# Kernel optimization log

Hardware: AMD Instinct MI355X
Metric: run time of the kernel (lower is better)

The kernel has to match this reference:

```python
import jax, jax.numpy as jnp
import numpy as np

N_NODES = 200000
E = 100000
H = 128            # hidden_dim = memory_dim = time_dim
EF = 64            # edge_feat_dim (raw_msg_dim)
L = 50             # price_seq_dim
LH = 32            # LSTM hidden size
MSG_DIM = EF + 2 * H + H  # IdentityMessage output = 448
N_PARTIES, N_STATES = 8, 56


def setup_inputs() -> dict:
    key = jax.random.key(0)
    ks = jax.random.split(key, 32)
    f = lambda k, shp, s=0.05: jax.random.normal(k, shp, dtype=jnp.float32) * s
    return {
        "src": jax.random.randint(ks[0], (E,), 0, N_NODES),
        "dst": jax.random.randint(ks[1], (E,), 0, N_NODES),
        "t": jnp.sort(jax.random.randint(ks[2], (E,), 0, 1000000)),
        "msg": jax.random.normal(ks[3], (E, EF), dtype=jnp.float32),
        "price_seq": jax.random.normal(ks[4], (E, L), dtype=jnp.float32),
        "trade_t": jax.random.randint(ks[5], (E,), 0, 1000000),
        "x_static": jax.random.randint(ks[6], (N_NODES, 2), 0, N_PARTIES),
        # TGN memory state
        "memory": f(ks[7], (N_NODES, H), 0.1),
        "last_update": jax.random.uniform(ks[8], (N_NODES,), dtype=jnp.float32) * 1000.0,
        # time encoder: cos(Linear(dt))
        "w_t": f(ks[9], (H,), 0.01),
        "b_t": f(ks[10], (H,)),
        # GRUCell memory updater
        "W_ih": f(ks[11], (3 * H, MSG_DIM)),
        "b_ih": f(ks[12], (3 * H,)),
        "W_hh": f(ks[13], (3 * H, H)),
        "b_hh": f(ks[14], (3 * H,)),
        # static embeddings + projection
        "party_emb": f(ks[15], (N_PARTIES, 16), 1.0),
        "state_emb": f(ks[16], (N_STATES, 16), 1.0),
        "W_sp": f(ks[17], (H, 32)),
        "b_sp": f(ks[18], (H,)),
        # price LSTM (input_size=1, hidden=32)
        "W_ih_l": f(ks[19], (4 * LH, 1)),
        "W_hh_l": f(ks[20], (4 * LH, LH)),
        "b_ih_l": f(ks[21], (4 * LH,)),
        "b_hh_l": f(ks[22], (4 * LH,)),
        "W_pp": f(ks[23], (H, LH)),
        "b_pp": f(ks[24], (H,)),
        # predictor MLP (dropout inactive at inference)
        "W1": f(ks[25], (64, 3 * H)),
        "b1": f(ks[26], (64,)),
        "W2": f(ks[27], (1, 64)),
        "b2": f(ks[28], (1,)),
    }


def reference(src, dst, t, msg, price_seq, trade_t, x_static, memory, last_update,
              w_t, b_t, W_ih, b_ih, W_hh, b_hh, party_emb, state_emb, W_sp, b_sp,
              W_ih_l, W_hh_l, b_ih_l, b_hh_l, W_pp, b_pp, W1, b1, W2, b2):
    N, Hd = memory.shape
    tf = t.astype(jnp.float32)
    t_enc = lambda dt: jnp.cos(dt[:, None] * w_t[None, :] + b_t[None, :])

    # ---- TGNMemory.update_state: gather -> message -> last-aggregate -> GRU scatter ----
    mem_s, mem_d = memory[src], memory[dst]
    msg_s = jnp.concatenate([mem_s, mem_d, msg, t_enc(tf - last_update[src])], axis=-1)
    msg_d = jnp.concatenate([mem_d, mem_s, msg, t_enc(tf - last_update[dst])], axis=-1)
    msgs = jnp.concatenate([msg_s, msg_d], axis=0)        # [2E, MSG_DIM]
    idx = jnp.concatenate([src, dst])                     # [2E]
    te = jnp.concatenate([tf, tf])
    M = idx.shape[0]
    # LastAggregator: per node, keep the message with the largest t (ties -> later event)
    perm = jnp.argsort(te)                                # stable ascending
    ranks = jnp.zeros((M,), jnp.int32).at[perm].set(jnp.arange(M, dtype=jnp.int32))
    win_rank = jax.ops.segment_max(ranks, idx, num_segments=N)  # int32 min for empty segs
    has_msg = win_rank >= 0
    win = perm[jnp.clip(win_rank, 0, M - 1)]
    agg = jnp.where(has_msg[:, None], msgs[win], 0.0)     # [N, MSG_DIM]
    # GRUCell update (applied only to nodes with messages)
    gi = agg @ W_ih.T + b_ih
    gh = memory @ W_hh.T + b_hh
    ir, iz, inn = jnp.split(gi, 3, axis=-1)
    hr, hz, hn = jnp.split(gh, 3, axis=-1)
    r = jax.nn.sigmoid(ir + hr)
    z = jax.nn.sigmoid(iz + hz)
    n = jnp.tanh(inn + r * hn)
    mem_new = jnp.where(has_msg[:, None], (1.0 - z) * n + z * memory, memory)

    # ---- static embeddings ----
    sf = jnp.concatenate([party_emb[x_static[src, 0]], state_emb[x_static[src, 1]]], axis=1)
    src_static = sf @ W_sp.T + b_sp

    # ---- price LSTM (input_size=1) ----
    B = price_seq.shape[0]
    nLH = W_hh_l.shape[1]
    bias = b_ih_l + b_hh_l

    def step(carry, x_t):
        h, c = carry
        g = x_t[:, None] * W_ih_l[:, 0][None, :] + h @ W_hh_l.T + bias
        i, fg, gg, o = jnp.split(g, 4, axis=-1)
        c = jax.nn.sigmoid(fg) * c + jax.nn.sigmoid(i) * jnp.tanh(gg)
        h = jax.nn.sigmoid(o) * jnp.tanh(c)
        return (h, c), None

    h0 = jnp.zeros((B, nLH), price_seq.dtype)
    (h_n, _), _ = jax.lax.scan(step, (h0, h0), price_seq.T)
    price_emb = h_n @ W_pp.T + b_pp

    # ---- fuse contexts + predictor MLP (dropout = identity at eval) ----
    combined = jnp.concatenate([mem_new[src] + src_static,
                                mem_new[dst] + price_emb,
                                price_emb], axis=1)
    h1 = jax.nn.relu(combined @ W1.T + b1)
    return (h1 @ W2.T + b2)[:, 0]
```

## Files before the change

### kernel.cpp

```cpp
#include <hip/hip_runtime.h>
#include <stdint.h>

#define NN    200000
#define NE    100000
#define HD    128
#define EFD   64
#define NG    384

typedef unsigned long long u64;
typedef short bf16x8 __attribute__((ext_vector_type(8)));
typedef float f32x4  __attribute__((ext_vector_type(4)));

#define OFF_KEY   ((size_t)0)
#define OFF_CNT   ((size_t)1600000)
#define OFF_LIST  ((size_t)1600256)
#define OFF_UV    ((size_t)2400256)
#define OFF_HN    ((size_t)104800256)
#define OFF_A     ((size_t)117600256)
#define OFF_B     ((size_t)117608448)
#define OFF_C0    ((size_t)117616640)
#define OFF_WBF   ((size_t)117616896)
#define WS_NEED   ((size_t)118092032)

#define W1OFF 221184

__device__ __forceinline__ float frcp(float x){ return __builtin_amdgcn_rcpf(x); }
__device__ __forceinline__ float sigf(float x){ return frcp(1.f + __expf(-x)); }
__device__ __forceinline__ float tanhf_(float x){ return 1.f - 2.f*frcp(__expf(2.f*x) + 1.f); }
__device__ __forceinline__ float4 ld4(const float* p){ return *reinterpret_cast<const float4*>(p); }

__device__ __forceinline__ short f2bf(float f){
  unsigned u = __float_as_uint(f);
  u += 0x7fffu + ((u>>16)&1u);
  return (short)(u>>16);
}

__device__ __forceinline__ unsigned cvtpk(float lo, float hi){
  unsigned r;
  asm("v_cvt_pk_bf16_f32 %0, %1, %2" : "=v"(r) : "v"(lo), "v"(hi));
  return r;
}

__device__ __forceinline__ void gl16(const void* g, void* l) {
  __builtin_amdgcn_global_load_lds(
      (const __attribute__((address_space(1))) void*)g,
      (__attribute__((address_space(3))) void*)l, 16, 0, 0);
}

__global__ void k_scatter(const int* __restrict__ src, const int* __restrict__ dst,
                          const int* __restrict__ t, u64* __restrict__ key) {
  int e = blockIdx.x*256 + threadIdx.x;
  if (e >= NE) return;
  u64 tt = (u64)(unsigned)(t[e] + 1);
  atomicMax(&key[src[e]], (tt<<18) | (u64)(unsigned)e);
  atomicMax(&key[dst[e]], (tt<<18) | (1ULL<<17) | (u64)(unsigned)e);
}

__global__ void k_compact(const u64* __restrict__ key, int* __restrict__ list,
                          int* __restrict__ count) {
  int n = blockIdx.x*256 + threadIdx.x;
  if (n >= NN) return;
  if (key[n] != 0ULL) { int p = atomicAdd(count, 1); list[p] = n; }
}

__global__ void k_pre(const float* __restrict__ W1, const float* __restrict__ W_sp,
                      const float* __restrict__ W_pp, const float* __restrict__ b_sp,
                      const float* __restrict__ b_pp, const float* __restrict__ b1,
                      float* __restrict__ A, float* __restrict__ B, float* __restrict__ c0)
{
  int tid = blockIdx.x*256 + threadIdx.x;
  if (tid < 2048) {
    int o = tid >> 5, j = tid & 31;
    float s = 0.f;
    for (int k = 0; k < 128; ++k) s = fmaf(W1[o*NG + k], W_sp[k*32 + j], s);
    A[tid] = s;
  } else if (tid < 4096) {
    int q = tid - 2048;
    int o = q >> 5, j = q & 31;
    float s = 0.f;
    for (int k = 0; k < 128; ++k)
      s = fmaf(W1[o*NG + 128 + k] + W1[o*NG + 256 + k], W_pp[k*32 + j], s);
    B[q] = s;
  } else if (tid < 4160) {
    int o = tid - 4096;
    float s = b1[o];
    for (int k = 0; k < 128; ++k) {
      s = fmaf(W1[o*NG + k], b_sp[k], s);
      s = fmaf(W1[o*NG + 128 + k] + W1[o*NG + 256 + k], b_pp[k], s);
    }
    c0[o] = s;
  }
}

__global__ void k_prew(const float* __restrict__ W_ih, const float* __restrict__ W_hh,
                       const float* __restrict__ W1, short* __restrict__ Wbf)
{
  int idx = blockIdx.x*256 + threadIdx.x;
  if (idx < 9*384*8) {
    int s   = idx & 7;
    int n   = (idx >> 3) % 384;
    int ch9 = idx / (384*8);
    int k8  = s ^ (n & 7);
    int k   = ch9*64 + k8*8;
    short v[8];
    #pragma unroll
    for (int e = 0; e < 8; ++e) {
      int kk = k + e;
      float f = (kk < 448) ? W_ih[(size_t)n*448 + kk] : W_hh[(size_t)n*HD + (kk-448)];
      v[e] = f2bf(f);
    }
    *reinterpret_cast<bf16x8*>(Wbf + (size_t)ch9*24576 + n*64 + s*8) =
        *reinterpret_cast<bf16x8*>(v);
  } else if (idx < 9*384*8 + 128*16) {
    int idx2 = idx - 9*384*8;
    int s = idx2 & 15, r = idx2 >> 4;
    int k8 = s ^ (r & 15);
    int k = k8*8;
    short v[8];
    #pragma unroll
    for (int e = 0; e < 8; ++e) {
      int kk = k + e;
      float f = (r < 64) ? W1[(size_t)r*NG + kk] : W1[(size_t)(r-64)*NG + 128 + kk];
      v[e] = f2bf(f);
    }
    *reinterpret_cast<bf16x8*>(Wbf + W1OFF + r*128 + s*8) =
        *reinterpret_cast<bf16x8*>(v);
  }
}

__global__ __launch_bounds__(512, 2) void k_gru(
    const u64* __restrict__ key, const int* __restrict__ list, const int* __restrict__ count,
    const int* __restrict__ src, const int* __restrict__ dst, const int* __restrict__ t,
    const float* __restrict__ msg, const float* __restrict__ memory,
    const float* __restrict__ last_update,
    const float* __restrict__ w_t, const float* __restrict__ b_t,
    const short* __restrict__ Wbf, const float* __restrict__ b_ih,
    const float* __restrict__ b_hh, float* __restrict__ uv)
{
  __shared__ short Wsb[24576];
  __shared__ short Xsb[4096];
  __shared__ float bias4[512];
  __shared__ int   sn_self[64];
  __shared__ int   sn_other[64];
  __shared__ int   sn_e[64];
  __shared__ float sn_dt[64];

  short* Mn2 = &Wsb[16384];

  int cnt = count[0];
  int base = blockIdx.x * 64;
  if (base >= cnt) return;
  int tid = threadIdx.x;
  int wid = tid >> 6, lane = tid & 63;
  int lr = lane & 15, lk = lane >> 4;

  if (tid < 64) {
    int idx = base + tid;
    int cl = idx < cnt ? idx : (cnt - 1);
    int n = list[cl];
    u64 k = key[n];
    int e   = (int)(k & 0x1FFFFULL);
    int isd = (int)((k >> 17) & 1ULL);
    sn_self[tid]  = n;
    sn_other[tid] = isd ? src[e] : dst[e];
    sn_e[tid]     = e;
    sn_dt[tid]    = (float)t[e] - last_update[n];
  }
  if (tid < 128) {
    int h = tid;
    bias4[h]       = b_ih[h]       + b_hh[h];
    bias4[128 + h] = b_ih[128 + h] + b_hh[128 + h];
    bias4[256 + h] = b_ih[256 + h];
    bias4[384 + h] = b_hh[256 + h];
  }
  __syncthreads();

  f32x4 aR[4], aZ[4], aNX[4], aNM[4];
  #pragma unroll
  for (int mt = 0; mt < 4; ++mt) { aR[mt] = (f32x4)0.f; aZ[mt] = (f32x4)0.f;
                                   aNX[mt] = (f32x4)0.f; aNM[mt] = (f32x4)0.f; }

  int node8 = tid >> 3, k8s = tid & 7;

  float4 xA0, xB0, xA1, xB1, xA2, xB2, xA3, xB3, xA4, xB4;
  {
    const float* pSelf  = memory + (size_t)sn_self[node8]*HD  + k8s*8;
    const float* pOther = memory + (size_t)sn_other[node8]*HD + k8s*8;
    const float* pMsg   = msg + (size_t)sn_e[node8]*EFD + k8s*8;
    xA0 = ld4(pSelf);       xB0 = ld4(pSelf+4);
    xA1 = ld4(pSelf+64);    xB1 = ld4(pSelf+68);
    xA2 = ld4(pOther);      xB2 = ld4(pOther+4);
    xA3 = ld4(pOther+64);   xB3 = ld4(pOther+68);
    xA4 = ld4(pMsg);        xB4 = ld4(pMsg+4);
  }

  constexpr int WCH[9] = {0, 7, 1, 8, 2, 3, 4, 5, 6};
  constexpr int XST[9] = {0,-1, 1,-1, 2, 3, 4,-2,-2};

  int hrow = wid*16 + lr;
  int swzH = (hrow & 7);

  #pragma unroll
  for (int p = 0; p < 9; ++p) {
    const int W = WCH[p];
    #pragma unroll
    for (int i = 0; i < 6; ++i) {
      int q = i*512 + tid;
      gl16(Wbf + (size_t)W*24576 + q*8, &Wsb[q*8]);
    }
    if (XST[p] >= 0) {
      float4 fa, fb;
      switch (XST[p]) {
        case 0: fa = xA0; fb = xB0; break;
        case 1: fa = xA1; fb = xB1; break;
        case 2: fa = xA2; fb = xB2; break;
        case 3: fa = xA3; fb = xB3; break;
        default: fa = xA4; fb = xB4; break;
      }
      short xs[8];
      xs[0]=f2bf(fa.x); xs[1]=f2bf(fa.y); xs[2]=f2bf(fa.z); xs[3]=f2bf(fa.w);
      xs[4]=f2bf(fb.x); xs[5]=f2bf(fb.y); xs[6]=f2bf(fb.z); xs[7]=f2bf(fb.w);
      *reinterpret_cast<bf16x8*>(&Xsb[node8*64 + ((k8s ^ (node8&7))<<3)]) =
          *reinterpret_cast<bf16x8*>(xs);
    } else if (XST[p] == -2) {
      int kk = (W == 6 ? 64 : 0) + k8s*8;
      float dt = sn_dt[node8];
      short xs[8];
      #pragma unroll
      for (int q = 0; q < 8; ++q) xs[q] = f2bf(cosf(fmaf(dt, w_t[kk+q], b_t[kk+q])));
      *reinterpret_cast<bf16x8*>(&Xsb[node8*64 + ((k8s ^ (node8&7))<<3)]) =
          *reinterpret_cast<bf16x8*>(xs);
    }
    __syncthreads();

    #pragma unroll
    for (int ks = 0; ks < 2; ++ks) {
      int k8 = ks*4 + lk;
      int so = (k8 ^ swzH) << 3;
      bf16x8 bR = *reinterpret_cast<const bf16x8*>(&Wsb[(size_t)hrow*64 + so]);
      bf16x8 bZ = *reinterpret_cast<const bf16x8*>(&Wsb[(size_t)(128+hrow)*64 + so]);
      bf16x8 bN = *reinterpret_cast<const bf16x8*>(&Wsb[(size_t)(256+hrow)*64 + so]);
      #pragma unroll
      for (int mt = 0; mt < 4; ++mt) {
        int anode = mt*16 + lr;
        bf16x8 a = *reinterpret_cast<const bf16x8*>(&Xsb[anode*64 + ((k8 ^ (anode&7))<<3)]);
        aR[mt] = __builtin_amdgcn_mfma_f32_16x16x32_bf16(a, bR, aR[mt], 0, 0, 0);
        aZ[mt] = __builtin_amdgcn_mfma_f32_16x16x32_bf16(a, bZ, aZ[mt], 0, 0, 0);
        if (W < 7) aNX[mt] = __builtin_amdgcn_mfma_f32_16x16x32_bf16(a, bN, aNX[mt], 0, 0, 0);
        else       aNM[mt] = __builtin_amdgcn_mfma_f32_16x16x32_bf16(a, bN, aNM[mt], 0, 0, 0);
      }
    }
    __syncthreads();
  }

  #pragma unroll
  for (int i = 0; i < 4; ++i) {
    int q = i*512 + tid;
    gl16(Wbf + W1OFF + q*8, &Wsb[q*8]);
  }

  {
    int h = hrow;
    int k8h = h >> 3, eh = h & 7;
    float br_ = bias4[h], bz_ = bias4[128+h], bnx_ = bias4[256+h], bnm_ = bias4[384+h];
    #pragma unroll
    for (int mt = 0; mt < 4; ++mt) {
      #pragma unroll
      for (int i = 0; i < 4; ++i) {
        int node = mt*16 + lk*4 + i;
        float r  = sigf(aR[mt][i] + br_);
        float z  = sigf(aZ[mt][i] + bz_);
        float nv = tanhf_(aNX[mt][i] + bnx_ + r*(aNM[mt][i] + bnm_));
        float m  = memory[(size_t)sn_self[node]*HD + h];
        Mn2[node*128 + ((k8h ^ (node&15))<<3) + eh] = f2bf((1.f - z)*nv + z*m);
      }
    }
  }
  __syncthreads();

  {
    int orow = wid*16 + lr;
    f32x4 acc2[4];
    #pragma unroll
    for (int mt = 0; mt < 4; ++mt) acc2[mt] = (f32x4)0.f;
    #pragma unroll
    for (int kf = 0; kf < 4; ++kf) {
      int k8 = kf*4 + lk;
      bf16x8 b = *reinterpret_cast<const bf16x8*>(&Wsb[orow*128 + ((k8 ^ (orow&15))<<3)]);
      #pragma unroll
      for (int mt = 0; mt < 4; ++mt) {
        int anode = mt*16 + lr;
        bf16x8 a = *reinterpret_cast<const bf16x8*>(&Mn2[anode*128 + ((k8 ^ (anode&15))<<3)]);
        acc2[mt] = __builtin_amdgcn_mfma_f32_16x16x32_bf16(a, b, acc2[mt], 0, 0, 0);
      }
    }
    #pragma unroll
    for (int mt = 0; mt < 4; ++mt) {
      #pragma unroll
      for (int i = 0; i < 4; ++i) {
        int node = mt*16 + lk*4 + i;
        if (base + node < cnt)
          uv[(size_t)sn_self[node]*128 + orow] = acc2[mt][i];
      }
    }
  }
}

__global__ __launch_bounds__(256) void k_lstm(
    const float* __restrict__ price, const float* __restrict__ W_ihl,
    const float* __restrict__ W_hhl, const float* __restrict__ b_ihl,
    const float* __restrict__ b_hhl, float* __restrict__ hn_out)
{
  __shared__ short Wb[4096];
  __shared__ float ps[64*50];
  __shared__ float hbuf[4][576];
  int tid = threadIdx.x;
  int lane = tid & 63, wid = tid >> 6;
  int lr = lane & 15, lk = lane >> 4;

  {
    int base = tid * 16;
    #pragma unroll
    for (int q = 0; q < 8; ++q) {
      unsigned pk = cvtpk(W_hhl[base + q*2], W_hhl[base + q*2 + 1]);
      reinterpret_cast<unsigned*>(Wb)[tid*8 + q] = pk;
    }
  }
  int ebase = blockIdx.x * 64;
  int m = NE - ebase; if (m > 64) m = 64;
  for (int i = tid; i < 64*50; i += 256) {
    int r = i / 50, cidx = i % 50;
    int rr = r < m ? r : m - 1;
    ps[i] = price[(size_t)(ebase + rr)*50 + cidx];
  }
  __syncthreads();

  bf16x8 bw[8];
  float wih8[8], bias8[8];
  #pragma unroll
  for (int t = 0; t < 8; ++t) {
    int row = t*16 + lr;
    bw[t] = *reinterpret_cast<const bf16x8*>(&Wb[row*32 + lk*8]);
    wih8[t] = W_ihl[row];
    bias8[t] = b_ihl[row] + b_hhl[row];
  }

  int we = wid * 16;
  float* hb = hbuf[wid];

  float c8[4][2];
  #pragma unroll
  for (int i = 0; i < 4; ++i) { c8[i][0] = 0.f; c8[i][1] = 0.f; }
  bf16x8 afrag = {0,0,0,0,0,0,0,0};

  #pragma unroll 1
  for (int s = 0; s < 50; ++s) {
    float xv[4];
    #pragma unroll
    for (int i = 0; i < 4; ++i) xv[i] = ps[(we + lk*4 + i)*50 + s];
    f32x4 acc[8];
    #pragma unroll
    for (int t = 0; t < 8; ++t) {
      f32x4 ci;
      #pragma unroll
      for (int i = 0; i < 4; ++i) ci[i] = fmaf(xv[i], wih8[t], bias8[t]);
      acc[t] = __builtin_amdgcn_mfma_f32_16x16x32_bf16(afrag, bw[t], ci, 0, 0, 0);
    }
    #pragma unroll
    for (int i = 0; i < 4; ++i) {
      #pragma unroll
      for (int p = 0; p < 2; ++p) {
        float ei = __expf(-acc[0+p][i]);
        float ef = __expf(-acc[2+p][i]);
        float eg = __expf(2.f*acc[4+p][i]);
        float eo = __expf(-acc[6+p][i]);
        float di = 1.f + ei, df_ = 1.f + ef, dg = eg + 1.f, do_ = 1.f + eo;
        float m1 = di*df_, m2 = do_*dg;
        float R  = frcp(m1*m2);
        float ig = R*df_*m2;
        float fg = R*di*m2;
        float og = R*m1*dg;
        float gg = fmaf(-2.f, R*m1*do_, 1.f);
        c8[i][p] = fmaf(fg, c8[i][p], ig*gg);
        float th = 1.f - 2.f*frcp(__expf(2.f*c8[i][p]) + 1.f);
        hb[(lk*4 + i)*36 + p*16 + lr] = og*th;
      }
    }
    asm volatile("s_waitcnt lgkmcnt(0)" ::: "memory");
    float4 h0 = *reinterpret_cast<const float4*>(&hb[lr*36 + lk*8]);
    float4 h1 = *reinterpret_cast<const float4*>(&hb[lr*36 + lk*8 + 4]);
    unsigned pk_[4];
    pk_[0] = cvtpk(h0.x, h0.y);
    pk_[1] = cvtpk(h0.z, h0.w);
    pk_[2] = cvtpk(h1.x, h1.y);
    pk_[3] = cvtpk(h1.z, h1.w);
    afrag = *reinterpret_cast<bf16x8*>(pk_);
  }

  int e_g = ebase + we + lr;
  if (e_g < NE) {
    float4 h0 = *reinterpret_cast<const float4*>(&hb[lr*36 + lk*8]);
    float4 h1 = *reinterpret_cast<const float4*>(&hb[lr*36 + lk*8 + 4]);
    *reinterpret_cast<float4*>(hn_out + (size_t)e_g*32 + lk*8)     = h0;
    *reinterpret_cast<float4*>(hn_out + (size_t)e_g*32 + lk*8 + 4) = h1;
  }
}

__global__ __launch_bounds__(256) void k_final(
    const int* __restrict__ src, const int* __restrict__ dst, const int* __restrict__ xst,
    const float* __restrict__ party, const float* __restrict__ state,
    const float* __restrict__ uv, const float* __restrict__ hn,
    const float* __restrict__ A, const float* __restrict__ B, const float* __restrict__ c0,
    const float* __restrict__ W2, const float* __restrict__ b2, float* __restrict__ out)
{
  __shared__ float As[2048], Bs[2048], c0s[64], W2s[64];
  int tid = threadIdx.x;
  for (int i = tid; i < 2048; i += 256) { As[i] = A[i]; Bs[i] = B[i]; }
  if (tid < 64) { c0s[tid] = c0[tid]; W2s[tid] = W2[tid]; }
  __syncthreads();
  int e = blockIdx.x*256 + tid;
  if (e >= NE) return;
  int s = src[e], d = dst[e];
  int p = xst[2*s], stt = xst[2*s + 1];
  float4 sf4[8], hv4[8];
  #pragma unroll
  for (int i = 0; i < 4; ++i) sf4[i]   = ld4(party + p*16 + i*4);
  #pragma unroll
  for (int i = 0; i < 4; ++i) sf4[4+i] = ld4(state + stt*16 + i*4);
  #pragma unroll
  for (int i = 0; i < 8; ++i) hv4[i] = ld4(hn + (size_t)e*32 + i*4);
  const float* urow = uv + (size_t)s*128;
  const float* vrow = uv + (size_t)d*128 + 64;
  float oacc = b2[0];
  #pragma unroll 4
  for (int o4 = 0; o4 < 16; ++o4) {
    float4 u4 = ld4(urow + o4*4);
    float4 v4 = ld4(vrow + o4*4);
    float4 cc = *reinterpret_cast<const float4*>(&c0s[o4*4]);
    float4 w2 = *reinterpret_cast<const float4*>(&W2s[o4*4]);
    float hh[4] = {u4.x+v4.x+cc.x, u4.y+v4.y+cc.y, u4.z+v4.z+cc.z, u4.w+v4.w+cc.w};
    #pragma unroll
    for (int oo = 0; oo < 4; ++oo) {
      int o = o4*4 + oo;
      float acc = hh[oo];
      #pragma unroll
      for (int j4 = 0; j4 < 8; ++j4) {
        float4 a = *reinterpret_cast<const float4*>(&As[o*32 + j4*4]);
        float4 b = *reinterpret_cast<const float4*>(&Bs[o*32 + j4*4]);
        float4 sfv = sf4[j4], hvv = hv4[j4];
        acc = fmaf(a.x,sfv.x, fmaf(a.y,sfv.y, fmaf(a.z,sfv.z, fmaf(a.w,sfv.w, acc))));
        acc = fmaf(b.x,hvv.x, fmaf(b.y,hvv.y, fmaf(b.z,hvv.z, fmaf(b.w,hvv.w, acc))));
      }
      float w2v = (oo==0) ? w2.x : (oo==1) ? w2.y : (oo==2) ? w2.z : w2.w;
      oacc = fmaf(w2v, fmaxf(acc, 0.f), oacc);
    }
  }
  out[e] = oacc;
}

extern "C" void kernel_launch(void* const* d_in, const int* in_sizes, int n_in,
                              void* d_out, int out_size, void* d_ws, size_t ws_size,
                              hipStream_t stream) {
  const int*   src   = (const int*)d_in[0];
  const int*   dst   = (const int*)d_in[1];
  const int*   t     = (const int*)d_in[2];
  const float* msg   = (const float*)d_in[3];
  const float* price = (const float*)d_in[4];
  const int*   xst   = (const int*)d_in[6];
  const float* memory= (const float*)d_in[7];
  const float* lu    = (const float*)d_in[8];
  const float* w_t   = (const float*)d_in[9];
  const float* b_t   = (const float*)d_in[10];
  const float* W_ih  = (const float*)d_in[11];
  const float* b_ih  = (const float*)d_in[12];
  const float* W_hh  = (const float*)d_in[13];
  const float* b_hh  = (const float*)d_in[14];
  const float* party = (const float*)d_in[15];
  const float* state = (const float*)d_in[16];
  const float* W_sp  = (const float*)d_in[17];
  const float* b_sp  = (const float*)d_in[18];
  const float* W_ihl = (const float*)d_in[19];
  const float* W_hhl = (const float*)d_in[20];
  const float* b_ihl = (const float*)d_in[21];
  const float* b_hhl = (const float*)d_in[22];
  const float* W_pp  = (const float*)d_in[23];
  const float* b_pp  = (const float*)d_in[24];
  const float* W1    = (const float*)d_in[25];
  const float* b1    = (const float*)d_in[26];
  const float* W2    = (const float*)d_in[27];
  const float* b2    = (const float*)d_in[28];
  float* out = (float*)d_out;

  if (ws_size < WS_NEED) {
    (void)hipMemsetAsync(d_out, 0, (size_t)out_size*4, stream);
    return;
  }

  char* ws = (char*)d_ws;
  u64*   key  = (u64*)(ws + OFF_KEY);
  int*   cnt  = (int*)(ws + OFF_CNT);
  int*   list = (int*)(ws + OFF_LIST);
  float* uv   = (float*)(ws + OFF_UV);
  float* hn   = (float*)(ws + OFF_HN);
  float* A    = (float*)(ws + OFF_A);
  float* B    = (float*)(ws + OFF_B);
  float* c0   = (float*)(ws + OFF_C0);
  short* Wbf  = (short*)(ws + OFF_WBF);

  (void)hipMemsetAsync(ws, 0, OFF_LIST, stream);
  k_scatter<<<(NE+255)/256, 256, 0, stream>>>(src, dst, t, key);
  k_compact<<<(NN+255)/256, 256, 0, stream>>>(key, list, cnt);
  k_pre<<<17, 256, 0, stream>>>(W1, W_sp, W_pp, b_sp, b_pp, b1, A, B, c0);
  k_prew<<<116, 256, 0, stream>>>(W_ih, W_hh, W1, Wbf);
  k_lstm<<<(NE+63)/64, 256, 0, stream>>>(price, W_ihl, W_hhl, b_ihl, b_hhl, hn);
  k_gru<<<(NN+63)/64, 512, 0, stream>>>(key, list, cnt, src, dst, t, msg, memory, lu,
                                        w_t, b_t, Wbf, b_ih, b_hh, uv);
  k_final<<<(NE+255)/256, 256, 0, stream>>>(src, dst, xst, party, state, uv, hn,
                                            A, B, c0, W2, b2, out);
}
```

Measured before the change: 523.7 us.

## Fuse GRU memory update and price LSTM into one interleaved launch

Merges the separate GRU-update and price-LSTM kernels into a single kernel. Block IDs are interleaved so every fifth block runs the LSTM, which now handles 128 edges with 512 threads, while the other four run the GRU tile. The LDS is shared through one raw byte buffer. The aim is to overlap the latency-bound sequential LSTM with the MFMA and gather-heavy GRU work and to drop one launch. The cost is that both paths now share the same register and LDS budget and the same launch bounds, which may reduce occupancy for the LSTM path.

```diff
diff --git a/kernel.cpp b/kernel.cpp
--- a/kernel.cpp
+++ b/kernel.cpp
@@ -23,6 +23,8 @@
 #define WS_NEED   ((size_t)118092032)
 
 #define W1OFF 221184
+#define GRUB  3128
+#define LSTB  782
 
 __device__ __forceinline__ float frcp(float x){ return __builtin_amdgcn_rcpf(x); }
 __device__ __forceinline__ float sigf(float x){ return frcp(1.f + __expf(-x)); }
@@ -34,13 +36,11 @@
   u += 0x7fffu + ((u>>16)&1u);
   return (short)(u>>16);
 }
-
 __device__ __forceinline__ unsigned cvtpk(float lo, float hi){
   unsigned r;
   asm("v_cvt_pk_bf16_f32 %0, %1, %2" : "=v"(r) : "v"(lo), "v"(hi));
   return r;
 }
-
 __device__ __forceinline__ void gl16(const void* g, void* l) {
   __builtin_amdgcn_global_load_lds(
       (const __attribute__((address_space(1))) void*)g,
@@ -128,281 +128,282 @@
   }
 }
 
-__global__ __launch_bounds__(512, 2) void k_gru(
+__global__ __launch_bounds__(512, 2) void k_gl(
     const u64* __restrict__ key, const int* __restrict__ list, const int* __restrict__ count,
     const int* __restrict__ src, const int* __restrict__ dst, const int* __restrict__ t,
     const float* __restrict__ msg, const float* __restrict__ memory,
     const float* __restrict__ last_update,
     const float* __restrict__ w_t, const float* __restrict__ b_t,
     const short* __restrict__ Wbf, const float* __restrict__ b_ih,
-    const float* __restrict__ b_hh, float* __restrict__ uv)
-{
-  __shared__ short Wsb[24576];
-  __shared__ short Xsb[4096];
-  __shared__ float bias4[512];
-  __shared__ int   sn_self[64];
-  __shared__ int   sn_other[64];
-  __shared__ int   sn_e[64];
-  __shared__ float sn_dt[64];
-
-  short* Mn2 = &Wsb[16384];
-
-  int cnt = count[0];
-  int base = blockIdx.x * 64;
-  if (base >= cnt) return;
-  int tid = threadIdx.x;
-  int wid = tid >> 6, lane = tid & 63;
-  int lr = lane & 15, lk = lane >> 4;
-
-  if (tid < 64) {
-    int idx = base + tid;
-    int cl = idx < cnt ? idx : (cnt - 1);
-    int n = list[cl];
-    u64 k = key[n];
-    int e   = (int)(k & 0x1FFFFULL);
-    int isd = (int)((k >> 17) & 1ULL);
-    sn_self[tid]  = n;
-    sn_other[tid] = isd ? src[e] : dst[e];
-    sn_e[tid]     = e;
-    sn_dt[tid]    = (float)t[e] - last_update[n];
-  }
-  if (tid < 128) {
-    int h = tid;
-    bias4[h]       = b_ih[h]       + b_hh[h];
-    bias4[128 + h] = b_ih[128 + h] + b_hh[128 + h];
-    bias4[256 + h] = b_ih[256 + h];
-    bias4[384 + h] = b_hh[256 + h];
-  }
-  __syncthreads();
-
-  f32x4 aR[4], aZ[4], aNX[4], aNM[4];
-  #pragma unroll
-  for (int mt = 0; mt < 4; ++mt) { aR[mt] = (f32x4)0.f; aZ[mt] = (f32x4)0.f;
-                                   aNX[mt] = (f32x4)0.f; aNM[mt] = (f32x4)0.f; }
-
-  int node8 = tid >> 3, k8s = tid & 7;
-
-  float4 xA0, xB0, xA1, xB1, xA2, xB2, xA3, xB3, xA4, xB4;
-  {
-    const float* pSelf  = memory + (size_t)sn_self[node8]*HD  + k8s*8;
-    const float* pOther = memory + (size_t)sn_other[node8]*HD + k8s*8;
-    const float* pMsg   = msg + (size_t)sn_e[node8]*EFD + k8s*8;
-    xA0 = ld4(pSelf);       xB0 = ld4(pSelf+4);
-    xA1 = ld4(pSelf+64);    xB1 = ld4(pSelf+68);
-    xA2 = ld4(pOther);      xB2 = ld4(pOther+4);
-    xA3 = ld4(pOther+64);   xB3 = ld4(pOther+68);
-    xA4 = ld4(pMsg);        xB4 = ld4(pMsg+4);
-  }
-
-  constexpr int WCH[9] = {0, 7, 1, 8, 2, 3, 4, 5, 6};
-  constexpr int XST[9] = {0,-1, 1,-1, 2, 3, 4,-2,-2};
-
-  int hrow = wid*16 + lr;
-  int swzH = (hrow & 7);
-
-  #pragma unroll
-  for (int p = 0; p < 9; ++p) {
-    const int W = WCH[p];
-    #pragma unroll
-    for (int i = 0; i < 6; ++i) {
-      int q = i*512 + tid;
-      gl16(Wbf + (size_t)W*24576 + q*8, &Wsb[q*8]);
-    }
-    if (XST[p] >= 0) {
-      float4 fa, fb;
-      switch (XST[p]) {
-        case 0: fa = xA0; fb = xB0; break;
-        case 1: fa = xA1; fb = xB1; break;
-        case 2: fa = xA2; fb = xB2; break;
-        case 3: fa = xA3; fb = xB3; break;
-        default: fa = xA4; fb = xB4; break;
-      }
-      short xs[8];
-      xs[0]=f2bf(fa.x); xs[1]=f2bf(fa.y); xs[2]=f2bf(fa.z); xs[3]=f2bf(fa.w);
-      xs[4]=f2bf(fb.x); xs[5]=f2bf(fb.y); xs[6]=f2bf(fb.z); xs[7]=f2bf(fb.w);
-      *reinterpret_cast<bf16x8*>(&Xsb[node8*64 + ((k8s ^ (node8&7))<<3)]) =
-          *reinterpret_cast<bf16x8*>(xs);
-    } else if (XST[p] == -2) {
-      int kk = (W == 6 ? 64 : 0) + k8s*8;
-      float dt = sn_dt[node8];
-      short xs[8];
-      #pragma unroll
-      for (int q = 0; q < 8; ++q) xs[q] = f2bf(cosf(fmaf(dt, w_t[kk+q], b_t[kk+q])));
-      *reinterpret_cast<bf16x8*>(&Xsb[node8*64 + ((k8s ^ (node8&7))<<3)]) =
-          *reinterpret_cast<bf16x8*>(xs);
-    }
-    __syncthreads();
-
-    #pragma unroll
-    for (int ks = 0; ks < 2; ++ks) {
-      int k8 = ks*4 + lk;
-      int so = (k8 ^ swzH) << 3;
-      bf16x8 bR = *reinterpret_cast<const bf16x8*>(&Wsb[(size_t)hrow*64 + so]);
-      bf16x8 bZ = *reinterpret_cast<const bf16x8*>(&Wsb[(size_t)(128+hrow)*64 + so]);
-      bf16x8 bN = *reinterpret_cast<const bf16x8*>(&Wsb[(size_t)(256+hrow)*64 + so]);
-      #pragma unroll
-      for (int mt = 0; mt < 4; ++mt) {
-        int anode = mt*16 + lr;
-        bf16x8 a = *reinterpret_cast<const bf16x8*>(&Xsb[anode*64 + ((k8 ^ (anode&7))<<3)]);
-        aR[mt] = __builtin_amdgcn_mfma_f32_16x16x32_bf16(a, bR, aR[mt], 0, 0, 0);
-        aZ[mt] = __builtin_amdgcn_mfma_f32_16x16x32_bf16(a, bZ, aZ[mt], 0, 0, 0);
-        if (W < 7) aNX[mt] = __builtin_amdgcn_mfma_f32_16x16x32_bf16(a, bN, aNX[mt], 0, 0, 0);
-        else       aNM[mt] = __builtin_amdgcn_mfma_f32_16x16x32_bf16(a, bN, aNM[mt], 0, 0, 0);
-      }
-    }
-    __syncthreads();
-  }
-
-  #pragma unroll
-  for (int i = 0; i < 4; ++i) {
-    int q = i*512 + tid;
-    gl16(Wbf + W1OFF + q*8, &Wsb[q*8]);
-  }
-
-  {
-    int h = hrow;
-    int k8h = h >> 3, eh = h & 7;
-    float br_ = bias4[h], bz_ = bias4[128+h], bnx_ = bias4[256+h], bnm_ = bias4[384+h];
-    #pragma unroll
-    for (int mt = 0; mt < 4; ++mt) {
-      #pragma unroll
-      for (int i = 0; i < 4; ++i) {
-        int node = mt*16 + lk*4 + i;
-        float r  = sigf(aR[mt][i] + br_);
-        float z  = sigf(aZ[mt][i] + bz_);
-        float nv = tanhf_(aNX[mt][i] + bnx_ + r*(aNM[mt][i] + bnm_));
-        float m  = memory[(size_t)sn_self[node]*HD + h];
-        Mn2[node*128 + ((k8h ^ (node&15))<<3) + eh] = f2bf((1.f - z)*nv + z*m);
-      }
-    }
-  }
-  __syncthreads();
-
-  {
-    int orow = wid*16 + lr;
-    f32x4 acc2[4];
-    #pragma unroll
-    for (int mt = 0; mt < 4; ++mt) acc2[mt] = (f32x4)0.f;
-    #pragma unroll
-    for (int kf = 0; kf < 4; ++kf) {
-      int k8 = kf*4 + lk;
-      bf16x8 b = *reinterpret_cast<const bf16x8*>(&Wsb[orow*128 + ((k8 ^ (orow&15))<<3)]);
-      #pragma unroll
-      for (int mt = 0; mt < 4; ++mt) {
-        int anode = mt*16 + lr;
-        bf16x8 a = *reinterpret_cast<const bf16x8*>(&Mn2[anode*128 + ((k8 ^ (anode&15))<<3)]);
-        acc2[mt] = __builtin_amdgcn_mfma_f32_16x16x32_bf16(a, b, acc2[mt], 0, 0, 0);
-      }
-    }
-    #pragma unroll
-    for (int mt = 0; mt < 4; ++mt) {
-      #pragma unroll
-      for (int i = 0; i < 4; ++i) {
-        int node = mt*16 + lk*4 + i;
-        if (base + node < cnt)
-          uv[(size_t)sn_self[node]*128 + orow] = acc2[mt][i];
-      }
-    }
-  }
-}
-
-__global__ __launch_bounds__(256) void k_lstm(
+    const float* __restrict__ b_hh, float* __restrict__ uv,
     const float* __restrict__ price, const float* __restrict__ W_ihl,
     const float* __restrict__ W_hhl, const float* __restrict__ b_ihl,
     const float* __restrict__ b_hhl, float* __restrict__ hn_out)
 {
-  __shared__ short Wb[4096];
-  __shared__ float ps[64*50];
-  __shared__ float hbuf[4][576];
+  __shared__ char lds[60416];
+  int bid = blockIdx.x;
   int tid = threadIdx.x;
-  int lane = tid & 63, wid = tid >> 6;
+  int wid = tid >> 6, lane = tid & 63;
   int lr = lane & 15, lk = lane >> 4;
 
-  {
-    int base = tid * 16;
-    #pragma unroll
-    for (int q = 0; q < 8; ++q) {
-      unsigned pk = cvtpk(W_hhl[base + q*2], W_hhl[base + q*2 + 1]);
-      reinterpret_cast<unsigned*>(Wb)[tid*8 + q] = pk;
-    }
-  }
-  int ebase = blockIdx.x * 64;
-  int m = NE - ebase; if (m > 64) m = 64;
-  for (int i = tid; i < 64*50; i += 256) {
-    int r = i / 50, cidx = i % 50;
-    int rr = r < m ? r : m - 1;
-    ps[i] = price[(size_t)(ebase + rr)*50 + cidx];
-  }
-  __syncthreads();
-
-  bf16x8 bw[8];
-  float wih8[8], bias8[8];
-  #pragma unroll
-  for (int t = 0; t < 8; ++t) {
-    int row = t*16 + lr;
-    bw[t] = *reinterpret_cast<const bf16x8*>(&Wb[row*32 + lk*8]);
-    wih8[t] = W_ihl[row];
-    bias8[t] = b_ihl[row] + b_hhl[row];
-  }
-
-  int we = wid * 16;
-  float* hb = hbuf[wid];
-
-  float c8[4][2];
-  #pragma unroll
-  for (int i = 0; i < 4; ++i) { c8[i][0] = 0.f; c8[i][1] = 0.f; }
-  bf16x8 afrag = {0,0,0,0,0,0,0,0};
-
-  #pragma unroll 1
-  for (int s = 0; s < 50; ++s) {
-    float xv[4];
-    #pragma unroll
-    for (int i = 0; i < 4; ++i) xv[i] = ps[(we + lk*4 + i)*50 + s];
-    f32x4 acc[8];
-    #pragma unroll
-    for (int t = 0; t < 8; ++t) {
-      f32x4 ci;
-      #pragma unroll
-      for (int i = 0; i < 4; ++i) ci[i] = fmaf(xv[i], wih8[t], bias8[t]);
-      acc[t] = __builtin_amdgcn_mfma_f32_16x16x32_bf16(afrag, bw[t], ci, 0, 0, 0);
-    }
+  if (bid % 5 != 4) {
+    int g = (bid/5)*4 + (bid%5);
+    short* Wsb   = reinterpret_cast<short*>(lds);
+    short* Xsb   = reinterpret_cast<short*>(lds + 49152);
+    float* bias4 = reinterpret_cast<float*>(lds + 57344);
+    int*   sn_self  = reinterpret_cast<int*>(lds + 59392);
+    int*   sn_other = reinterpret_cast<int*>(lds + 59648);
+    int*   sn_e     = reinterpret_cast<int*>(lds + 59904);
+    float* sn_dt    = reinterpret_cast<float*>(lds + 60160);
+    short* Mn2 = &Wsb[16384];
+
+    int cnt = count[0];
+    int base = g * 64;
+    if (base >= cnt) return;
+
+    if (tid < 64) {
+      int idx = base + tid;
+      int cl = idx < cnt ? idx : (cnt - 1);
+      int n = list[cl];
+      u64 k = key[n];
+      int e   = (int)(k & 0x1FFFFULL);
+      int isd = (int)((k >> 17) & 1ULL);
+      sn_self[tid]  = n;
+      sn_other[tid] = isd ? src[e] : dst[e];
+      sn_e[tid]     = e;
+      sn_dt[tid]    = (float)t[e] - last_update[n];
+    }
+    if (tid < 128) {
+      int h = tid;
+      bias4[h]       = b_ih[h]       + b_hh[h];
+      bias4[128 + h] = b_ih[128 + h] + b_hh[128 + h];
+      bias4[256 + h] = b_ih[256 + h];
+      bias4[384 + h] = b_hh[256 + h];
+    }
+    __syncthreads();
+
+    f32x4 aR[4], aZ[4], aNX[4], aNM[4];
+    #pragma unroll
+    for (int mt = 0; mt < 4; ++mt) { aR[mt] = (f32x4)0.f; aZ[mt] = (f32x4)0.f;
+                                     aNX[mt] = (f32x4)0.f; aNM[mt] = (f32x4)0.f; }
+
+    int node8 = tid >> 3, k8s = tid & 7;
+
+    float4 xA0, xB0, xA1, xB1, xA2, xB2, xA3, xB3, xA4, xB4;
+    {
+      const float* pSelf  = memory + (size_t)sn_self[node8]*HD  + k8s*8;
+      const float* pOther = memory + (size_t)sn_other[node8]*HD + k8s*8;
+      const float* pMsg   = msg + (size_t)sn_e[node8]*EFD + k8s*8;
+      xA0 = ld4(pSelf);       xB0 = ld4(pSelf+4);
+      xA1 = ld4(pSelf+64);    xB1 = ld4(pSelf+68);
+      xA2 = ld4(pOther);      xB2 = ld4(pOther+4);
+      xA3 = ld4(pOther+64);   xB3 = ld4(pOther+68);
+      xA4 = ld4(pMsg);        xB4 = ld4(pMsg+4);
+    }
+
+    constexpr int WCH[9] = {0, 7, 1, 8, 2, 3, 4, 5, 6};
+    constexpr int XST[9] = {0,-1, 1,-1, 2, 3, 4,-2,-2};
+
+    int hrow = wid*16 + lr;
+    int swzH = (hrow & 7);
+
+    #pragma unroll
+    for (int p = 0; p < 9; ++p) {
+      const int W = WCH[p];
+      #pragma unroll
+      for (int i = 0; i < 6; ++i) {
+        int q = i*512 + tid;
+        gl16(Wbf + (size_t)W*24576 + q*8, &Wsb[q*8]);
+      }
+      if (XST[p] >= 0) {
+        float4 fa, fb;
+        switch (XST[p]) {
+          case 0: fa = xA0; fb = xB0; break;
+          case 1: fa = xA1; fb = xB1; break;
+          case 2: fa = xA2; fb = xB2; break;
+          case 3: fa = xA3; fb = xB3; break;
+          default: fa = xA4; fb = xB4; break;
+        }
+        short xs[8];
+        xs[0]=f2bf(fa.x); xs[1]=f2bf(fa.y); xs[2]=f2bf(fa.z); xs[3]=f2bf(fa.w);
+        xs[4]=f2bf(fb.x); xs[5]=f2bf(fb.y); xs[6]=f2bf(fb.z); xs[7]=f2bf(fb.w);
+        *reinterpret_cast<bf16x8*>(&Xsb[node8*64 + ((k8s ^ (node8&7))<<3)]) =
+            *reinterpret_cast<bf16x8*>(xs);
+      } else if (XST[p] == -2) {
+        int kk = (W == 6 ? 64 : 0) + k8s*8;
+        float dt = sn_dt[node8];
+        short xs[8];
+        #pragma unroll
+        for (int q = 0; q < 8; ++q) xs[q] = f2bf(cosf(fmaf(dt, w_t[kk+q], b_t[kk+q])));
+        *reinterpret_cast<bf16x8*>(&Xsb[node8*64 + ((k8s ^ (node8&7))<<3)]) =
+            *reinterpret_cast<bf16x8*>(xs);
+      }
+      __syncthreads();
+
+      #pragma unroll
+      for (int ks = 0; ks < 2; ++ks) {
+        int k8 = ks*4 + lk;
+        int so = (k8 ^ swzH) << 3;
+        bf16x8 bR = *reinterpret_cast<const bf16x8*>(&Wsb[(size_t)hrow*64 + so]);
+        bf16x8 bZ = *reinterpret_cast<const bf16x8*>(&Wsb[(size_t)(128+hrow)*64 + so]);
+        bf16x8 bN = *reinterpret_cast<const bf16x8*>(&Wsb[(size_t)(256+hrow)*64 + so]);
+        #pragma unroll
+        for (int mt = 0; mt < 4; ++mt) {
+          int anode = mt*16 + lr;
+          bf16x8 a = *reinterpret_cast<const bf16x8*>(&Xsb[anode*64 + ((k8 ^ (anode&7))<<3)]);
+          aR[mt] = __builtin_amdgcn_mfma_f32_16x16x32_bf16(a, bR, aR[mt], 0, 0, 0);
+          aZ[mt] = __builtin_amdgcn_mfma_f32_16x16x32_bf16(a, bZ, aZ[mt], 0, 0, 0);
+          if (W < 7) aNX[mt] = __builtin_amdgcn_mfma_f32_16x16x32_bf16(a, bN, aNX[mt], 0, 0, 0);
+          else       aNM[mt] = __builtin_amdgcn_mfma_f32_16x16x32_bf16(a, bN, aNM[mt], 0, 0, 0);
+        }
+      }
+      __syncthreads();
+    }
+
     #pragma unroll
     for (int i = 0; i < 4; ++i) {
-      #pragma unroll
-      for (int p = 0; p < 2; ++p) {
-        float ei = __expf(-acc[0+p][i]);
-        float ef = __expf(-acc[2+p][i]);
-        float eg = __expf(2.f*acc[4+p][i]);
-        float eo = __expf(-acc[6+p][i]);
-        float di = 1.f + ei, df_ = 1.f + ef, dg = eg + 1.f, do_ = 1.f + eo;
-        float m1 = di*df_, m2 = do_*dg;
-        float R  = frcp(m1*m2);
-        float ig = R*df_*m2;
-        float fg = R*di*m2;
-        float og = R*m1*dg;
-        float gg = fmaf(-2.f, R*m1*do_, 1.f);
-        c8[i][p] = fmaf(fg, c8[i][p], ig*gg);
-        float th = 1.f - 2.f*frcp(__expf(2.f*c8[i][p]) + 1.f);
-        hb[(lk*4 + i)*36 + p*16 + lr] = og*th;
-      }
-    }
-    asm volatile("s_waitcnt lgkmcnt(0)" ::: "memory");
-    float4 h0 = *reinterpret_cast<const float4*>(&hb[lr*36 + lk*8]);
-    float4 h1 = *reinterpret_cast<const float4*>(&hb[lr*36 + lk*8 + 4]);
-    unsigned pk_[4];
-    pk_[0] = cvtpk(h0.x, h0.y);
-    pk_[1] = cvtpk(h0.z, h0.w);
-    pk_[2] = cvtpk(h1.x, h1.y);
-    pk_[3] = cvtpk(h1.z, h1.w);
-    afrag = *reinterpret_cast<bf16x8*>(pk_);
-  }
-
-  int e_g = ebase + we + lr;
-  if (e_g < NE) {
-    float4 h0 = *reinterpret_cast<const float4*>(&hb[lr*36 + lk*8]);
-    float4 h1 = *reinterpret_cast<const float4*>(&hb[lr*36 + lk*8 + 4]);
-    *reinterpret_cast<float4*>(hn_out + (size_t)e_g*32 + lk*8)     = h0;
-    *reinterpret_cast<float4*>(hn_out + (size_t)e_g*32 + lk*8 + 4) = h1;
+      int q = i*512 + tid;
+      gl16(Wbf + W1OFF + q*8, &Wsb[q*8]);
+    }
+
+    {
+      int h = hrow;
+      int k8h = h >> 3, eh = h & 7;
+      float br_ = bias4[h], bz_ = bias4[128+h], bnx_ = bias4[256+h], bnm_ = bias4[384+h];
+      #pragma unroll
+      for (int mt = 0; mt < 4; ++mt) {
+        #pragma unroll
+        for (int i = 0; i < 4; ++i) {
+          int node = mt*16 + lk*4 + i;
+          float r  = sigf(aR[mt][i] + br_);
+          float z  = sigf(aZ[mt][i] + bz_);
+          float nv = tanhf_(aNX[mt][i] + bnx_ + r*(aNM[mt][i] + bnm_));
+          float m  = memory[(size_t)sn_self[node]*HD + h];
+          Mn2[node*128 + ((k8h ^ (node&15))<<3) + eh] = f2bf((1.f - z)*nv + z*m);
+        }
+      }
+    }
+    __syncthreads();
+
+    {
+      int orow = wid*16 + lr;
+      f32x4 acc2[4];
+      #pragma unroll
+      for (int mt = 0; mt < 4; ++mt) acc2[mt] = (f32x4)0.f;
+      #pragma unroll
+      for (int kf = 0; kf < 4; ++kf) {
+        int k8 = kf*4 + lk;
+        bf16x8 b = *reinterpret_cast<const bf16x8*>(&Wsb[orow*128 + ((k8 ^ (orow&15))<<3)]);
+        #pragma unroll
+        for (int mt = 0; mt < 4; ++mt) {
+          int anode = mt*16 + lr;
+          bf16x8 a = *reinterpret_cast<const bf16x8*>(&Mn2[anode*128 + ((k8 ^ (anode&15))<<3)]);
+          acc2[mt] = __builtin_amdgcn_mfma_f32_16x16x32_bf16(a, b, acc2[mt], 0, 0, 0);
+        }
+      }
+      #pragma unroll
+      for (int mt = 0; mt < 4; ++mt) {
+        #pragma unroll
+        for (int i = 0; i < 4; ++i) {
+          int node = mt*16 + lk*4 + i;
+          if (base + node < cnt)
+            uv[(size_t)sn_self[node]*128 + orow] = acc2[mt][i];
+        }
+      }
+    }
+  } else {
+    int l = bid / 5;
+    if (l >= LSTB) return;
+    short* Wb   = reinterpret_cast<short*>(lds);
+    float* ps   = reinterpret_cast<float*>(lds + 8192);
+    float* hbuf = reinterpret_cast<float*>(lds + 33792);
+
+    {
+      int base = tid * 8;
+      #pragma unroll
+      for (int q = 0; q < 4; ++q) {
+        unsigned pk = cvtpk(W_hhl[base + q*2], W_hhl[base + q*2 + 1]);
+        reinterpret_cast<unsigned*>(Wb)[tid*4 + q] = pk;
+      }
+    }
+    int ebase = l * 128;
+    int m = NE - ebase; if (m > 128) m = 128;
+    for (int i = tid; i < 128*50; i += 512) {
+      int r = i / 50, cidx = i % 50;
+      int rr = r < m ? r : m - 1;
+      ps[i] = price[(size_t)(ebase + rr)*50 + cidx];
+    }
+    __syncthreads();
+
+    bf16x8 bw[8];
+    float wih8[8], bias8[8];
+    #pragma unroll
+    for (int tI = 0; tI < 8; ++tI) {
+      int row = tI*16 + lr;
+      bw[tI] = *reinterpret_cast<const bf16x8*>(&Wb[row*32 + lk*8]);
+      wih8[tI] = W_ihl[row];
+      bias8[tI] = b_ihl[row] + b_hhl[row];
+    }
+
+    int we = wid * 16;
+    float* hb = hbuf + wid*576;
+
+    float c8[4][2];
+    #pragma unroll
+    for (int i = 0; i < 4; ++i) { c8[i][0] = 0.f; c8[i][1] = 0.f; }
+    bf16x8 afrag = {0,0,0,0,0,0,0,0};
+
+    #pragma unroll 1
+    for (int s = 0; s < 50; ++s) {
+      float xv[4];
+      #pragma unroll
+      for (int i = 0; i < 4; ++i) xv[i] = ps[(we + lk*4 + i)*50 + s];
+      f32x4 acc[8];
+      #pragma unroll
+      for (int tI = 0; tI < 8; ++tI) {
+        f32x4 ci;
+        #pragma unroll
+        for (int i = 0; i < 4; ++i) ci[i] = fmaf(xv[i], wih8[tI], bias8[tI]);
+        acc[tI] = __builtin_amdgcn_mfma_f32_16x16x32_bf16(afrag, bw[tI], ci, 0, 0, 0);
+      }
+      #pragma unroll
+      for (int i = 0; i < 4; ++i) {
+        #pragma unroll
+        for (int p = 0; p < 2; ++p) {
+          float ei = __expf(-acc[0+p][i]);
+          float ef = __expf(-acc[2+p][i]);
+          float eg = __expf(2.f*acc[4+p][i]);
+          float eo = __expf(-acc[6+p][i]);
+          float di = 1.f + ei, df_ = 1.f + ef, dg = eg + 1.f, do_ = 1.f + eo;
+          float m1 = di*df_, m2 = do_*dg;
+          float R  = frcp(m1*m2);
+          float ig = R*df_*m2;
+          float fg = R*di*m2;
+          float og = R*m1*dg;
+          float gg = fmaf(-2.f, R*m1*do_, 1.f);
+          c8[i][p] = fmaf(fg, c8[i][p], ig*gg);
+          float th = 1.f - 2.f*frcp(__expf(2.f*c8[i][p]) + 1.f);
+          hb[(lk*4 + i)*36 + p*16 + lr] = og*th;
+        }
+      }
+      asm volatile("s_waitcnt lgkmcnt(0)" ::: "memory");
+      float4 h0 = *reinterpret_cast<const float4*>(&hb[lr*36 + lk*8]);
+      float4 h1 = *reinterpret_cast<const float4*>(&hb[lr*36 + lk*8 + 4]);
+      unsigned pk_[4];
+      pk_[0] = cvtpk(h0.x, h0.y);
+      pk_[1] = cvtpk(h0.z, h0.w);
+      pk_[2] = cvtpk(h1.x, h1.y);
+      pk_[3] = cvtpk(h1.z, h1.w);
+      afrag = *reinterpret_cast<bf16x8*>(pk_);
+    }
+
+    int e_g = ebase + we + lr;
+    if (e_g < NE) {
+      float4 h0 = *reinterpret_cast<const float4*>(&hb[lr*36 + lk*8]);
+      float4 h1 = *reinterpret_cast<const float4*>(&hb[lr*36 + lk*8 + 4]);
+      *reinterpret_cast<float4*>(hn_out + (size_t)e_g*32 + lk*8)     = h0;
+      *reinterpret_cast<float4*>(hn_out + (size_t)e_g*32 + lk*8 + 4) = h1;
+    }
   }
 }
 
@@ -512,9 +513,9 @@
   k_compact<<<(NN+255)/256, 256, 0, stream>>>(key, list, cnt);
   k_pre<<<17, 256, 0, stream>>>(W1, W_sp, W_pp, b_sp, b_pp, b1, A, B, c0);
   k_prew<<<116, 256, 0, stream>>>(W_ih, W_hh, W1, Wbf);
-  k_lstm<<<(NE+63)/64, 256, 0, stream>>>(price, W_ihl, W_hhl, b_ihl, b_hhl, hn);
-  k_gru<<<(NN+63)/64, 512, 0, stream>>>(key, list, cnt, src, dst, t, msg, memory, lu,
-                                        w_t, b_t, Wbf, b_ih, b_hh, uv);
+  k_gl<<<LSTB*5, 512, 0, stream>>>(key, list, cnt, src, dst, t, msg, memory, lu,
+                                   w_t, b_t, Wbf, b_ih, b_hh, uv,
+                                   price, W_ihl, W_hhl, b_ihl, b_hhl, hn);
   k_final<<<(NE+255)/256, 256, 0, stream>>>(src, dst, xst, party, state, uv, hn,
                                             A, B, c0, W2, b2, out);
 }
```

After: 475.6 us. 9.2% less time.
